# Kernel tuning notes

Measured on AMD Instinct MI355X. Metric: run time of the kernel, lower is better.

## Reference

```python
import jax, jax.numpy as jnp
import numpy as np

NEG_BIG = -9e15

def setup_inputs() -> dict:
    key = jax.random.key(0)
    k1, k2, k3, k4 = jax.random.split(key, 4)
    N, Fin, Fout = 8192, 256, 128
    x = jax.random.normal(k1, (N, Fin), dtype=jnp.float32)
    adj = jax.random.randint(k2, (N, N), 0, 2, dtype=jnp.int32)
    # xavier-uniform-like init
    limW = float(np.sqrt(6.0 / (Fin + Fout)))
    W = jax.random.uniform(k3, (Fin, Fout), minval=-limW, maxval=limW, dtype=jnp.float32)
    lima = float(np.sqrt(6.0 / (2 * Fout + 1)))
    a = jax.random.uniform(k4, (2 * Fout, 1), minval=-lima, maxval=lima, dtype=jnp.float32)
    return {"x": x, "adj": adj, "W": W, "a": a}

def reference(x, adj, W, a, alpha=0.2):
    # h: (N, Fout)
    h = x @ W
    Fout = W.shape[1]
    # Split a into source/target halves: e[i,j] = leakyrelu(h_i·a1 + h_j·a2)
    a1, a2 = a[:Fout, 0], a[Fout:, 0]
    s = h @ a1  # (N,) row (source) scores
    t = h @ a2  # (N,) col (target) scores
    e = jax.nn.leaky_relu(s[:, None] + t[None, :], negative_slope=alpha)  # (N, N)
    e = jnp.where(adj > 0, e, NEG_BIG)
    attention = jax.nn.softmax(e, axis=1)
    # dropout omitted (eval mode / training=False)
    return attention @ h
```

## Files before the change

kernel.cpp:

```cpp
#include <hip/hip_runtime.h>
#include <hip/hip_bf16.h>

typedef __attribute__((ext_vector_type(8))) short short8;
typedef __attribute__((ext_vector_type(4))) short short4v;
typedef __attribute__((ext_vector_type(4))) float f32x4;

#define NR 8192
#define LOG2E 1.4426950408889634f

__device__ __forceinline__ short f2bf(float f) {
  return __builtin_bit_cast(short, __float2bfloat16(f));
}

__global__ __launch_bounds__(256) void k_gemm_h(const float* __restrict__ x,
                                                const float* __restrict__ W,
                                                const float* __restrict__ a,
                                                short* __restrict__ HT,
                                                float* __restrict__ sv,
                                                float* __restrict__ tv) {
  __shared__ short WT[128][136];
  const int tid = threadIdx.x;
  const int w = tid >> 6;
  const int L = tid & 63;
  const int lm = L & 15;
  const int q = L >> 4;
  const int i0 = blockIdx.x * 64;

  f32x4 acc[8];
#pragma unroll
  for (int nn = 0; nn < 8; ++nn) acc[nn] = (f32x4){0.f, 0.f, 0.f, 0.f};

  for (int kc = 0; kc < 256; kc += 128) {
    if (kc) __syncthreads();
#pragma unroll
    for (int p = 0; p < 16; ++p) {
      int idx = p * 256 + tid;
      int k = idx >> 5;
      int f4 = (idx & 31) * 4;
      float4 v = *(const float4*)&W[(kc + k) * 128 + f4];
      WT[f4 + 0][k] = f2bf(v.x);
      WT[f4 + 1][k] = f2bf(v.y);
      WT[f4 + 2][k] = f2bf(v.z);
      WT[f4 + 3][k] = f2bf(v.w);
    }
    __syncthreads();
#pragma unroll
    for (int ks = 0; ks < 4; ++ks) {
      int row = i0 + 16 * w + lm;
      const float* xp = &x[(size_t)row * 256 + kc + ks * 32 + q * 8];
      float4 xa = *(const float4*)xp;
      float4 xb = *(const float4*)(xp + 4);
      short8 af;
      af[0] = f2bf(xa.x); af[1] = f2bf(xa.y); af[2] = f2bf(xa.z); af[3] = f2bf(xa.w);
      af[4] = f2bf(xb.x); af[5] = f2bf(xb.y); af[6] = f2bf(xb.z); af[7] = f2bf(xb.w);
#pragma unroll
      for (int nn = 0; nn < 8; ++nn) {
        short8 bf = *(const short8*)&WT[nn * 16 + lm][ks * 32 + q * 8];
        acc[nn] = __builtin_amdgcn_mfma_f32_16x16x32_bf16(af, bf, acc[nn], 0, 0, 0);
      }
    }
  }

  const int ib = i0 + 16 * w + 4 * q;
  float a1v[8], a2v[8];
#pragma unroll
  for (int nn = 0; nn < 8; ++nn) {
    a1v[nn] = a[nn * 16 + lm];
    a2v[nn] = a[128 + nn * 16 + lm];
  }
  float sr[4] = {0.f, 0.f, 0.f, 0.f};
  float tr[4] = {0.f, 0.f, 0.f, 0.f};
#pragma unroll
  for (int nn = 0; nn < 8; ++nn) {
    int f = nn * 16 + lm;
    short4v o;
    o[0] = f2bf(acc[nn][0]);
    o[1] = f2bf(acc[nn][1]);
    o[2] = f2bf(acc[nn][2]);
    o[3] = f2bf(acc[nn][3]);
    *(short4v*)&HT[(size_t)f * NR + ib] = o;
#pragma unroll
    for (int r = 0; r < 4; ++r) {
      sr[r] += acc[nn][r] * a1v[nn];
      tr[r] += acc[nn][r] * a2v[nn];
    }
  }
#pragma unroll
  for (int d = 1; d < 16; d <<= 1) {
#pragma unroll
    for (int r = 0; r < 4; ++r) {
      sr[r] += __shfl_xor(sr[r], d);
      tr[r] += __shfl_xor(tr[r], d);
    }
  }
  if (lm == 0) {
#pragma unroll
    for (int r = 0; r < 4; ++r) {
      sv[ib + r] = sr[r] * LOG2E;
      tv[ib + r] = tr[r] * LOG2E;
    }
  }
}

__global__ __launch_bounds__(256, 3) void k_flash(const int* __restrict__ adj,
                                                  const short* __restrict__ HT,
                                                  const float* __restrict__ sv,
                                                  const float* __restrict__ tv,
                                                  float* __restrict__ part,
                                                  float* __restrict__ lpart,
                                                  int S) {
  const int tid = threadIdx.x;
  const int w = tid >> 6;
  const int L = tid & 63;
  const int lm = L & 15;
  const int q = L >> 4;
  const int sp = blockIdx.x >> 6;
  const int it = blockIdx.x & 63;
  const int i0 = it * 128;

  const int row0 = i0 + 32 * w + lm;
  const int row1 = row0 + 16;
  const float s0 = sv[row0];
  const float s1 = sv[row1];
  const size_t ar0 = (size_t)row0 * NR;
  const size_t ar1 = (size_t)row1 * NR;

  f32x4 acc[2][8];
#pragma unroll
  for (int mm = 0; mm < 2; ++mm)
#pragma unroll
    for (int nn = 0; nn < 8; ++nn) acc[mm][nn] = (f32x4){0.f, 0.f, 0.f, 0.f};
  float l0 = 0.f, l1 = 0.f;

  const int JR = NR / S;
  const int j0 = sp * JR;
  const int niter = JR >> 5;

#pragma unroll 2
  for (int jk = 0; jk < niter; ++jk) {
    const int jb = j0 + (jk << 5) + q * 8;
    float4 t0 = *(const float4*)&tv[jb];
    float4 t1 = *(const float4*)&tv[jb + 4];
    int4 a00 = *(const int4*)&adj[ar0 + jb];
    int4 a01 = *(const int4*)&adj[ar0 + jb + 4];
    int4 a10 = *(const int4*)&adj[ar1 + jb];
    int4 a11 = *(const int4*)&adj[ar1 + jb + 4];
    short8 bf[8];
#pragma unroll
    for (int nn = 0; nn < 8; ++nn)
      bf[nn] = *(const short8*)&HT[(size_t)(nn * 16 + lm) * NR + jb];

    float tvl[8] = {t0.x, t0.y, t0.z, t0.w, t1.x, t1.y, t1.z, t1.w};
    int av0[8] = {a00.x, a00.y, a00.z, a00.w, a01.x, a01.y, a01.z, a01.w};
    int av1[8] = {a10.x, a10.y, a10.z, a10.w, a11.x, a11.y, a11.z, a11.w};
    short8 p0, p1;
#pragma unroll
    for (int e = 0; e < 8; ++e) {
      float v0 = s0 + tvl[e];
      float e0 = fmaxf(v0, 0.2f * v0);
      float pp0 = (av0[e] > 0) ? __builtin_amdgcn_exp2f(e0) : 0.f;
      l0 += pp0;
      p0[e] = f2bf(pp0);
      float v1 = s1 + tvl[e];
      float e1 = fmaxf(v1, 0.2f * v1);
      float pp1 = (av1[e] > 0) ? __builtin_amdgcn_exp2f(e1) : 0.f;
      l1 += pp1;
      p1[e] = f2bf(pp1);
    }
#pragma unroll
    for (int nn = 0; nn < 8; ++nn) {
      acc[0][nn] = __builtin_amdgcn_mfma_f32_16x16x32_bf16(p0, bf[nn], acc[0][nn], 0, 0, 0);
      acc[1][nn] = __builtin_amdgcn_mfma_f32_16x16x32_bf16(p1, bf[nn], acc[1][nn], 0, 0, 0);
    }
  }

  float* ps = part + (size_t)sp * (NR * 128);
#pragma unroll
  for (int mm = 0; mm < 2; ++mm) {
    int ib = i0 + 32 * w + 16 * mm + 4 * q;
#pragma unroll
    for (int nn = 0; nn < 8; ++nn) {
      int f = nn * 16 + lm;
#pragma unroll
      for (int r = 0; r < 4; ++r) ps[(size_t)(ib + r) * 128 + f] = acc[mm][nn][r];
    }
  }
  l0 += __shfl_xor(l0, 16);
  l0 += __shfl_xor(l0, 32);
  l1 += __shfl_xor(l1, 16);
  l1 += __shfl_xor(l1, 32);
  if (q == 0) {
    lpart[sp * NR + row0] = l0;
    lpart[sp * NR + row1] = l1;
  }
}

__global__ __launch_bounds__(256) void k_reduce(const float* __restrict__ part,
                                                const float* __restrict__ lpart,
                                                float* __restrict__ out, int S) {
  int idx4 = blockIdx.x * 256 + threadIdx.x;
  int idx = idx4 * 4;
  int i = idx >> 7;
  float4 sum = {0.f, 0.f, 0.f, 0.f};
  for (int sp = 0; sp < S; ++sp) {
    float4 v = *(const float4*)&part[(size_t)sp * (NR * 128) + idx];
    sum.x += v.x; sum.y += v.y; sum.z += v.z; sum.w += v.w;
  }
  float l = 0.f;
  for (int sp = 0; sp < S; ++sp) l += lpart[sp * NR + i];
  float inv = (l > 0.f) ? 1.f / l : 0.f;
  float4 o = {sum.x * inv, sum.y * inv, sum.z * inv, sum.w * inv};
  *(float4*)&out[idx] = o;
}

extern "C" void kernel_launch(void* const* d_in, const int* in_sizes, int n_in,
                              void* d_out, int out_size, void* d_ws, size_t ws_size,
                              hipStream_t stream) {
  const float* x = (const float*)d_in[0];
  const int* adj = (const int*)d_in[1];
  const float* W = (const float*)d_in[2];
  const float* a = (const float*)d_in[3];
  float* out = (float*)d_out;

  char* ws = (char*)d_ws;
  short* HT = (short*)(ws + 0);
  float* sv = (float*)(ws + 2097152);
  float* tv = (float*)(ws + 2129920);
  float* lpart = (float*)(ws + 2162688);
  float* part = (float*)(ws + 3145728);

  int S = 16;
  while (S > 1 && (size_t)3145728 + (size_t)S * 4194304 > ws_size) S >>= 1;

  hipLaunchKernelGGL(k_gemm_h, dim3(128), dim3(256), 0, stream, x, W, a, HT, sv, tv);
  hipLaunchKernelGGL(k_flash, dim3(64 * S), dim3(256), 0, stream, adj, HT, sv, tv,
                     part, lpart, S);
  hipLaunchKernelGGL(k_reduce, dim3((NR * 128) / 1024), dim3(256), 0, stream, part,
                     lpart, out, S);
}
```

Before: 450.3 us.

## Pre-pack adjacency into a bitmask and read bits in the flash kernel

A new pre-pass kernel compresses the int32 adjacency matrix into one bit per entry, and the attention kernel reads 32-bit mask words instead of int4 adjacency vectors. Launch bounds are also raised to 4 blocks per CU. The goal is to shrink the memory stream and register use inside the compute-heavy flash loop. The full adjacency still has to be read once in the separate pass, so total traffic does not drop, and the mask now needs extra workspace.

New measurement: 565.5 us. +25.6%, slower.

```diff
diff --git a/kernel.cpp b/kernel.cpp
--- a/kernel.cpp
+++ b/kernel.cpp
@@ -10,6 +10,22 @@
 
 __device__ __forceinline__ short f2bf(float f) {
   return __builtin_bit_cast(short, __float2bfloat16(f));
+}
+
+__global__ __launch_bounds__(256) void k_pack(const int* __restrict__ adj,
+                                              unsigned* __restrict__ mask) {
+  size_t gid = (size_t)blockIdx.x * 256 + threadIdx.x;
+  const int4* p = (const int4*)&adj[gid * 32];
+  unsigned m = 0;
+#pragma unroll
+  for (int c = 0; c < 8; ++c) {
+    int4 v = p[c];
+    m |= (unsigned)(v.x > 0) << (c * 4 + 0);
+    m |= (unsigned)(v.y > 0) << (c * 4 + 1);
+    m |= (unsigned)(v.z > 0) << (c * 4 + 2);
+    m |= (unsigned)(v.w > 0) << (c * 4 + 3);
+  }
+  mask[gid] = m;
 }
 
 __global__ __launch_bounds__(256) void k_gemm_h(const float* __restrict__ x,
@@ -102,7 +118,7 @@
   }
 }
 
-__global__ __launch_bounds__(256, 3) void k_flash(const int* __restrict__ adj,
+__global__ __launch_bounds__(256, 4) void k_flash(const unsigned* __restrict__ mask,
                                                   const short* __restrict__ HT,
                                                   const float* __restrict__ sv,
                                                   const float* __restrict__ tv,
@@ -122,8 +138,6 @@
   const int row1 = row0 + 16;
   const float s0 = sv[row0];
   const float s1 = sv[row1];
-  const size_t ar0 = (size_t)row0 * NR;
-  const size_t ar1 = (size_t)row1 * NR;
 
   f32x4 acc[2][8];
 #pragma unroll
@@ -134,43 +148,48 @@
 
   const int JR = NR / S;
   const int j0 = sp * JR;
-  const int niter = JR >> 5;
+  const int ngroups = JR >> 7;
+  const int w0base = row0 * 256 + (j0 >> 5);
+  const int w1base = row1 * 256 + (j0 >> 5);
 
 #pragma unroll 2
-  for (int jk = 0; jk < niter; ++jk) {
-    const int jb = j0 + (jk << 5) + q * 8;
-    float4 t0 = *(const float4*)&tv[jb];
-    float4 t1 = *(const float4*)&tv[jb + 4];
-    int4 a00 = *(const int4*)&adj[ar0 + jb];
-    int4 a01 = *(const int4*)&adj[ar0 + jb + 4];
-    int4 a10 = *(const int4*)&adj[ar1 + jb];
-    int4 a11 = *(const int4*)&adj[ar1 + jb + 4];
-    short8 bf[8];
-#pragma unroll
-    for (int nn = 0; nn < 8; ++nn)
-      bf[nn] = *(const short8*)&HT[(size_t)(nn * 16 + lm) * NR + jb];
-
-    float tvl[8] = {t0.x, t0.y, t0.z, t0.w, t1.x, t1.y, t1.z, t1.w};
-    int av0[8] = {a00.x, a00.y, a00.z, a00.w, a01.x, a01.y, a01.z, a01.w};
-    int av1[8] = {a10.x, a10.y, a10.z, a10.w, a11.x, a11.y, a11.z, a11.w};
-    short8 p0, p1;
-#pragma unroll
-    for (int e = 0; e < 8; ++e) {
-      float v0 = s0 + tvl[e];
-      float e0 = fmaxf(v0, 0.2f * v0);
-      float pp0 = (av0[e] > 0) ? __builtin_amdgcn_exp2f(e0) : 0.f;
-      l0 += pp0;
-      p0[e] = f2bf(pp0);
-      float v1 = s1 + tvl[e];
-      float e1 = fmaxf(v1, 0.2f * v1);
-      float pp1 = (av1[e] > 0) ? __builtin_amdgcn_exp2f(e1) : 0.f;
-      l1 += pp1;
-      p1[e] = f2bf(pp1);
-    }
-#pragma unroll
-    for (int nn = 0; nn < 8; ++nn) {
-      acc[0][nn] = __builtin_amdgcn_mfma_f32_16x16x32_bf16(p0, bf[nn], acc[0][nn], 0, 0, 0);
-      acc[1][nn] = __builtin_amdgcn_mfma_f32_16x16x32_bf16(p1, bf[nn], acc[1][nn], 0, 0, 0);
+  for (int jg = 0; jg < ngroups; ++jg) {
+    uint4 mw0 = *(const uint4*)&mask[w0base + jg * 4];
+    uint4 mw1 = *(const uint4*)&mask[w1base + jg * 4];
+    unsigned mwa0[4] = {mw0.x, mw0.y, mw0.z, mw0.w};
+    unsigned mwa1[4] = {mw1.x, mw1.y, mw1.z, mw1.w};
+#pragma unroll
+    for (int jk = 0; jk < 4; ++jk) {
+      const int jb = j0 + (jg * 4 + jk) * 32 + q * 8;
+      float4 t0 = *(const float4*)&tv[jb];
+      float4 t1 = *(const float4*)&tv[jb + 4];
+      short8 bf[8];
+#pragma unroll
+      for (int nn = 0; nn < 8; ++nn)
+        bf[nn] = *(const short8*)&HT[(size_t)(nn * 16 + lm) * NR + jb];
+
+      const unsigned b0 = (mwa0[jk] >> (q * 8)) & 0xffu;
+      const unsigned b1 = (mwa1[jk] >> (q * 8)) & 0xffu;
+      float tvl[8] = {t0.x, t0.y, t0.z, t0.w, t1.x, t1.y, t1.z, t1.w};
+      short8 p0, p1;
+#pragma unroll
+      for (int e = 0; e < 8; ++e) {
+        float v0 = s0 + tvl[e];
+        float e0 = fmaxf(v0, 0.2f * v0);
+        float pp0 = (b0 & (1u << e)) ? __builtin_amdgcn_exp2f(e0) : 0.f;
+        l0 += pp0;
+        p0[e] = f2bf(pp0);
+        float v1 = s1 + tvl[e];
+        float e1 = fmaxf(v1, 0.2f * v1);
+        float pp1 = (b1 & (1u << e)) ? __builtin_amdgcn_exp2f(e1) : 0.f;
+        l1 += pp1;
+        p1[e] = f2bf(pp1);
+      }
+#pragma unroll
+      for (int nn = 0; nn < 8; ++nn) {
+        acc[0][nn] = __builtin_amdgcn_mfma_f32_16x16x32_bf16(p0, bf[nn], acc[0][nn], 0, 0, 0);
+        acc[1][nn] = __builtin_amdgcn_mfma_f32_16x16x32_bf16(p1, bf[nn], acc[1][nn], 0, 0, 0);
+      }
     }
   }
 
@@ -227,13 +246,15 @@
   float* sv = (float*)(ws + 2097152);
   float* tv = (float*)(ws + 2129920);
   float* lpart = (float*)(ws + 2162688);
-  float* part = (float*)(ws + 3145728);
+  unsigned* mask = (unsigned*)(ws + 2686976);
+  float* part = (float*)(ws + 11075584);
 
   int S = 16;
-  while (S > 1 && (size_t)3145728 + (size_t)S * 4194304 > ws_size) S >>= 1;
-
+  while (S > 1 && (size_t)11075584 + (size_t)S * 4194304 > ws_size) S >>= 1;
+
+  hipLaunchKernelGGL(k_pack, dim3((NR * NR / 32) / 256), dim3(256), 0, stream, adj, mask);
   hipLaunchKernelGGL(k_gemm_h, dim3(128), dim3(256), 0, stream, x, W, a, HT, sv, tv);
-  hipLaunchKernelGGL(k_flash, dim3(64 * S), dim3(256), 0, stream, adj, HT, sv, tv,
+  hipLaunchKernelGGL(k_flash, dim3(64 * S), dim3(256), 0, stream, mask, HT, sv, tv,
                      part, lpart, S);
   hipLaunchKernelGGL(k_reduce, dim3((NR * 128) / 1024), dim3(256), 0, stream, part,
                      lpart, out, S);
```
